# Optimization experiments

Hardware: AMD Instinct MI355X
Metric: run time of the kernel (lower is better)

The kernel has to match this reference:

```python
import jax, jax.numpy as jnp
import numpy as np

B, S, D, H, E, K = 4, 1024, 1024, 4096, 8, 2


def setup_inputs() -> dict:
    key = jax.random.key(0)
    ks = jax.random.split(key, 10)
    s = 0.02
    return {
        "x": jax.random.normal(ks[0], (B, S, D), jnp.float32),
        "noise": jax.random.normal(ks[1], (B, S, E), jnp.float32),
        "Wg": jax.random.normal(ks[2], (D, E), jnp.float32) * s,
        "bg": jnp.zeros((E,), jnp.float32),
        "Wn": jax.random.normal(ks[3], (D, E), jnp.float32) * s,
        "bn": jnp.zeros((E,), jnp.float32),
        "W1": jax.random.normal(ks[4], (E, D, H), jnp.float32) * s,
        "b1": jnp.zeros((E, H), jnp.float32),
        "W2": jax.random.normal(ks[5], (E, H, D), jnp.float32) * s,
        "b2": jnp.zeros((E, D), jnp.float32),
    }


def reference(x, noise, Wg, bg, Wn, bn, W1, b1, W2, b2):
    # --- noisy top-k gating ---
    logits = x @ Wg + bg                                   # [B,S,E]
    noisy = logits + noise * jax.nn.softplus(x @ Wn + bn)  # [B,S,E]
    topk_vals, topk_idx = jax.lax.top_k(noisy, K)          # [B,S,K]
    weights = jax.nn.softmax(topk_vals, axis=-1)           # [B,S,K]
    oh = jax.nn.one_hot(topk_idx, E, dtype=x.dtype)        # [B,S,K,E]
    mask = oh.sum(axis=-2)                                 # [B,S,E] 0/1 (topk idx distinct)
    w_full = (weights[..., None] * oh).sum(axis=-2)        # [B,S,E] combine weights

    # --- per-expert FFN (dense over experts, selected via w_full) ---
    h = jax.nn.gelu(jnp.einsum('bsd,edh->bseh', x, W1) + b1, approximate=False)
    eout = jnp.einsum('bseh,ehd->bsed', h, W2) + b2        # [B,S,E,D]
    combined = jnp.einsum('bse,bsed->bsd', w_full, eout)   # [B,S,D]

    # --- load balancing loss on clean gate probs ---
    gate_probs = jax.nn.softmax(logits, axis=-1)           # [B,S,E]
    expert_count = mask.sum(axis=(0, 1))                   # [E]
    total_tokens = mask.sum()
    expert_util = expert_count / total_tokens
    load_loss = jnp.sum(expert_util * gate_probs.mean(axis=(0, 1))) * E
    return combined, load_loss
```

## Files before the change

kernel.cpp:

```cpp
#include <hip/hip_runtime.h>
#include <hip/hip_bf16.h>

#define T_TOK 4096
#define D_DIM 1024
#define H_DIM 4096
#define E_EXP 8
#define K_TOP 2
#define TP (T_TOK * K_TOP)
#define BM 128
#define BN 128
#define BKS 32
#define MAX_TILES 72

typedef __attribute__((ext_vector_type(8))) short bf16x8;
typedef __attribute__((ext_vector_type(4))) float f32x4;
typedef __attribute__((ext_vector_type(8))) unsigned short u16x8;
typedef __attribute__((ext_vector_type(4))) unsigned short u16x4;

#define SWZ(row, chunk) ((chunk) ^ (((row) >> 1) & 3))

static __device__ __forceinline__ void gload16(const unsigned short* g, unsigned short* l) {
  __builtin_amdgcn_global_load_lds((const __attribute__((address_space(1))) void*)g,
                                   (__attribute__((address_space(3))) void*)l, 16, 0, 0);
}

static __device__ __forceinline__ unsigned short f2bf(float f) {
  unsigned int bits = __float_as_uint(f);
  unsigned int lsb = (bits >> 16) & 1u;
  bits += 0x7fffu + lsb;
  return (unsigned short)(bits >> 16);
}

static __device__ __forceinline__ float gelu_fast(float u) {
  float z = u * (0.79788456080286536f + 0.0356774081f * u * u);
  float t = __expf(-2.f * z);
  return u / (1.f + t);
}

__global__ __launch_bounds__(256) void transpose_bf16_kernel(
    const float* __restrict__ src, unsigned short* __restrict__ dst, int R, int C) {
  __shared__ float tile[64][65];
  const int e = blockIdx.z;
  const int c0 = blockIdx.x * 64, r0 = blockIdx.y * 64;
  const int tid = threadIdx.x;
  const float* s = src + (size_t)e * R * C;
  unsigned short* d = dst + (size_t)e * R * C;

  const int rr = tid >> 4, c4 = tid & 15;
#pragma unroll
  for (int p = 0; p < 4; ++p) {
    int r = rr + p * 16;
    float4 v = *(const float4*)(&s[(size_t)(r0 + r) * C + c0 + c4 * 4]);
    tile[r][c4 * 4 + 0] = v.x;
    tile[r][c4 * 4 + 1] = v.y;
    tile[r][c4 * 4 + 2] = v.z;
    tile[r][c4 * 4 + 3] = v.w;
  }
  __syncthreads();
  const int cc = tid >> 3, r8 = tid & 7;
#pragma unroll
  for (int p = 0; p < 2; ++p) {
    int c = cc + p * 32;
    u16x8 o;
#pragma unroll
    for (int q = 0; q < 8; ++q) o[q] = f2bf(tile[r8 * 8 + q][c]);
    *(u16x8*)(&d[(size_t)(c0 + c) * R + r0 + r8 * 8]) = o;
  }
}

__global__ __launch_bounds__(256) void gating_kernel(
    const float* __restrict__ x, const float* __restrict__ noise,
    const float* __restrict__ Wg, const float* __restrict__ bg,
    const float* __restrict__ Wn, const float* __restrict__ bn,
    int* __restrict__ tok_e, float* __restrict__ tok_w,
    float* __restrict__ gp_tok, int* __restrict__ counts,
    unsigned short* __restrict__ xb) {
  const int tid = threadIdx.x, lane = tid & 63, wid = tid >> 6;
  const int t = blockIdx.x * 4 + wid;
  const float* xrow = x + (size_t)t * D_DIM;
  float ag[8] = {0, 0, 0, 0, 0, 0, 0, 0};
  float an[8] = {0, 0, 0, 0, 0, 0, 0, 0};
#pragma unroll 4
  for (int i = 0; i < 16; ++i) {
    int dd = i * 64 + lane;
    float xv = xrow[dd];
    xb[(size_t)t * D_DIM + dd] = f2bf(xv);
    const float4* g4 = (const float4*)(Wg + (size_t)dd * 8);
    const float4* n4 = (const float4*)(Wn + (size_t)dd * 8);
    float4 ga = g4[0], gb = g4[1], na = n4[0], nb = n4[1];
    ag[0] += xv * ga.x; ag[1] += xv * ga.y; ag[2] += xv * ga.z; ag[3] += xv * ga.w;
    ag[4] += xv * gb.x; ag[5] += xv * gb.y; ag[6] += xv * gb.z; ag[7] += xv * gb.w;
    an[0] += xv * na.x; an[1] += xv * na.y; an[2] += xv * na.z; an[3] += xv * na.w;
    an[4] += xv * nb.x; an[5] += xv * nb.y; an[6] += xv * nb.z; an[7] += xv * nb.w;
  }
#pragma unroll
  for (int e = 0; e < 8; ++e) {
    for (int off = 32; off > 0; off >>= 1) {
      ag[e] += __shfl_down(ag[e], off);
      an[e] += __shfl_down(an[e], off);
    }
  }
  if (lane == 0) {
    float logit[8], noisy[8];
#pragma unroll
    for (int e = 0; e < 8; ++e) {
      logit[e] = ag[e] + bg[e];
      float pre = an[e] + bn[e];
      float sp = fmaxf(pre, 0.f) + log1pf(expf(-fabsf(pre)));
      noisy[e] = logit[e] + noise[(size_t)t * 8 + e] * sp;
    }
    float mx = logit[0];
#pragma unroll
    for (int e = 1; e < 8; ++e) mx = fmaxf(mx, logit[e]);
    float s = 0.f, p[8];
#pragma unroll
    for (int e = 0; e < 8; ++e) { p[e] = expf(logit[e] - mx); s += p[e]; }
    float inv = 1.f / s;
#pragma unroll
    for (int e = 0; e < 8; ++e) gp_tok[(size_t)t * 8 + e] = p[e] * inv;
    int i0 = 0; float v0 = noisy[0];
#pragma unroll
    for (int e = 1; e < 8; ++e) if (noisy[e] > v0) { v0 = noisy[e]; i0 = e; }
    int i1 = -1; float v1 = 0.f;
#pragma unroll
    for (int e = 0; e < 8; ++e) {
      if (e == i0) continue;
      if (i1 < 0 || noisy[e] > v1) { v1 = noisy[e]; i1 = e; }
    }
    float e1 = expf(v1 - v0);
    float w0 = 1.f / (1.f + e1);
    float w1 = e1 * w0;
    tok_e[t * 2 + 0] = i0; tok_e[t * 2 + 1] = i1;
    tok_w[t * 2 + 0] = w0; tok_w[t * 2 + 1] = w1;
    atomicAdd(&counts[i0], 1);
    atomicAdd(&counts[i1], 1);
  }
}

__global__ void scan_kernel(const int* __restrict__ counts, int* __restrict__ offsets,
                            int* __restrict__ cursor, int4* __restrict__ tiles,
                            int* __restrict__ ntiles) {
  if (threadIdx.x == 0 && blockIdx.x == 0) {
    int off = 0, nt = 0;
    for (int e = 0; e < E_EXP; ++e) {
      offsets[e] = off;
      int c = counts[e];
      for (int r = 0; r < c; r += BM) {
        tiles[nt] = make_int4(e, off + r, min(BM, c - r), 0);
        ++nt;
      }
      off += c;
      cursor[e] = 0;
    }
    offsets[E_EXP] = off;
    *ntiles = nt;
  }
}

__global__ __launch_bounds__(256) void scatter_kernel(
    const int* __restrict__ tok_e, const float* __restrict__ tok_w,
    const int* __restrict__ offsets, int* __restrict__ cursor,
    int* __restrict__ pair_token, float* __restrict__ pair_w) {
  int t = blockIdx.x * 256 + threadIdx.x;
  if (t >= T_TOK) return;
#pragma unroll
  for (int k = 0; k < 2; ++k) {
    int e = tok_e[t * 2 + k];
    int pos = atomicAdd(&cursor[e], 1);
    int p = offsets[e] + pos;
    pair_token[p] = t;
    pair_w[p] = tok_w[t * 2 + k];
  }
}

__global__ __launch_bounds__(256) void ffn1_kernel(
    const unsigned short* __restrict__ xb,
    const unsigned short* __restrict__ w1t,
    const float* __restrict__ b1,
    const int* __restrict__ pair_token,
    const int4* __restrict__ tiles, const int* __restrict__ ntiles,
    unsigned short* __restrict__ hbuf) {
  const int NB = H_DIM / BN;
  const int nwg = MAX_TILES * NB;
  int bid = blockIdx.x;
  int wg = (bid & 7) * (nwg >> 3) + (bid >> 3);
  int tileId = wg / NB, nb = wg - tileId * NB;
  if (tileId >= *ntiles) return;
  int4 tl = tiles[tileId];
  const int e = tl.x, row0 = tl.y, rows = tl.z;
  const int n0 = nb * BN;

  __shared__ unsigned short sh[16384];
#define AS1(buf) (sh + (buf) * 4096)
#define BS1(buf) (sh + 8192 + (buf) * 4096)

  const int tid = threadIdx.x;
  const int wid = tid >> 6, lane = tid & 63;
  const int sr = tid >> 2;
  const int sc = tid & 3;
  const int scz = SWZ(sr, sc) * 8;

  int r0a = row0 + sr;       if (r0a > TP - 1) r0a = TP - 1;
  int r1a = row0 + sr + 64;  if (r1a > TP - 1) r1a = TP - 1;
  const unsigned short* a0 = xb + (size_t)pair_token[r0a] * D_DIM + scz;
  const unsigned short* a1 = xb + (size_t)pair_token[r1a] * D_DIM + scz;
  const unsigned short* bp0 = w1t + ((size_t)e * H_DIM + (n0 + sr)) * D_DIM + scz;
  const unsigned short* bp1 = w1t + ((size_t)e * H_DIM + (n0 + sr + 64)) * D_DIM + scz;

  const int wbase = wid * 512;
  const int wr = wid >> 1, wc = wid & 1;
  const int lrow = lane & 15, lkc = lane >> 4;

  f32x4 acc[4][4] = {};

  auto stage = [&](int buf, int k0) {
    gload16(a0 + k0, AS1(buf) + wbase);
    gload16(a1 + k0, AS1(buf) + wbase + 2048);
    gload16(bp0 + k0, BS1(buf) + wbase);
    gload16(bp1 + k0, BS1(buf) + wbase + 2048);
  };
  auto compute_step = [&](int buf) {
    bf16x8 af[4], bfr[4];
#pragma unroll
    for (int m = 0; m < 4; ++m) {
      int r = wr * 64 + m * 16 + lrow;
      af[m] = *(const bf16x8*)(AS1(buf) + r * BKS + SWZ(r, lkc) * 8);
    }
#pragma unroll
    for (int n = 0; n < 4; ++n) {
      int r = wc * 64 + n * 16 + lrow;
      bfr[n] = *(const bf16x8*)(BS1(buf) + r * BKS + SWZ(r, lkc) * 8);
    }
#pragma unroll
    for (int m = 0; m < 4; ++m)
#pragma unroll
      for (int n = 0; n < 4; ++n)
        acc[m][n] = __builtin_amdgcn_mfma_f32_16x16x32_bf16(af[m], bfr[n], acc[m][n], 0, 0, 0);
  };

  const int NK = D_DIM / BKS;
  stage(0, 0);
  stage(1, BKS);
  int cur = 0;
  for (int k = 0; k < NK - 1; ++k) {
    asm volatile("s_waitcnt vmcnt(4)" ::: "memory");
    __builtin_amdgcn_s_barrier();
    __builtin_amdgcn_sched_barrier(0);
    compute_step(cur);
    __builtin_amdgcn_sched_barrier(0);
    __builtin_amdgcn_s_barrier();
    if (k < NK - 2) stage(cur, (k + 2) * BKS);
    cur ^= 1;
  }
  asm volatile("s_waitcnt vmcnt(0)" ::: "memory");
  __builtin_amdgcn_s_barrier();
  __builtin_amdgcn_sched_barrier(0);
  compute_step(cur);

  __syncthreads();
#pragma unroll
  for (int n = 0; n < 4; ++n) {
    int clocal = wc * 64 + n * 16 + lrow;
    float bias = b1[(size_t)e * H_DIM + n0 + clocal];
    int chunk = clocal >> 3, within = clocal & 7;
#pragma unroll
    for (int m = 0; m < 4; ++m) {
#pragma unroll
      for (int j = 0; j < 4; ++j) {
        int rloc = wr * 64 + m * 16 + (lane >> 4) * 4 + j;
        float v = acc[m][n][j] + bias;
        sh[rloc * 128 + ((chunk ^ ((rloc >> 1) & 7)) * 8) + within] = f2bf(gelu_fast(v));
      }
    }
  }
  __syncthreads();
#pragma unroll
  for (int it = 0; it < 8; ++it) {
    int u = tid + 256 * it;
    int r = u >> 4, cg = u & 15;
    if (r < rows) {
      u16x8 v = *(const u16x8*)(&sh[r * 128 + ((cg ^ ((r >> 1) & 7)) * 8)]);
      *(u16x8*)(&hbuf[(size_t)(row0 + r) * H_DIM + n0 + cg * 8]) = v;
    }
  }
#undef AS1
#undef BS1
}

__global__ __launch_bounds__(256) void ffn2_kernel(
    const unsigned short* __restrict__ hbuf,
    const unsigned short* __restrict__ w2t,
    const float* __restrict__ b2,
    const int* __restrict__ pair_token, const float* __restrict__ pair_w,
    const int4* __restrict__ tiles, const int* __restrict__ ntiles,
    float* __restrict__ out) {
  const int NB = D_DIM / BN;
  const int nwg = MAX_TILES * NB;
  int bid = blockIdx.x;
  int wg = (bid & 7) * (nwg >> 3) + (bid >> 3);
  int tileId = wg / NB, nb = wg - tileId * NB;
  if (tileId >= *ntiles) return;
  int4 tl = tiles[tileId];
  const int e = tl.x, row0 = tl.y, rows = tl.z;
  const int n0 = nb * BN;

  __shared__ unsigned short As[2][BM * BKS];
  __shared__ unsigned short Bs[2][BN * BKS];
  __shared__ int stok[BM];
  __shared__ float spw[BM];

  const int tid = threadIdx.x;
  if (tid < BM) {
    int rr = row0 + tid; if (rr > TP - 1) rr = TP - 1;
    stok[tid] = pair_token[rr];
    spw[tid] = pair_w[rr];
  }

  const int wid = tid >> 6, lane = tid & 63;
  const int sr = tid >> 2;
  const int sc = tid & 3;
  const int scz = SWZ(sr, sc) * 8;

  int r0a = row0 + sr;       if (r0a > TP - 1) r0a = TP - 1;
  int r1a = row0 + sr + 64;  if (r1a > TP - 1) r1a = TP - 1;
  const unsigned short* a0 = hbuf + (size_t)r0a * H_DIM + scz;
  const unsigned short* a1 = hbuf + (size_t)r1a * H_DIM + scz;
  const unsigned short* bp0 = w2t + ((size_t)e * D_DIM + (n0 + sr)) * H_DIM + scz;
  const unsigned short* bp1 = w2t + ((size_t)e * D_DIM + (n0 + sr + 64)) * H_DIM + scz;

  const int wbase = wid * 512;
  const int wr = wid >> 1, wc = wid & 1;
  const int lrow = lane & 15, lkc = lane >> 4;

  f32x4 acc[4][4] = {};

  auto stage = [&](int buf, int k0) {
    gload16(a0 + k0, &As[buf][wbase]);
    gload16(a1 + k0, &As[buf][wbase + 2048]);
    gload16(bp0 + k0, &Bs[buf][wbase]);
    gload16(bp1 + k0, &Bs[buf][wbase + 2048]);
  };
  auto compute_step = [&](int buf) {
    bf16x8 af[4], bfr[4];
#pragma unroll
    for (int m = 0; m < 4; ++m) {
      int r = wr * 64 + m * 16 + lrow;
      af[m] = *(const bf16x8*)(&As[buf][r * BKS + SWZ(r, lkc) * 8]);
    }
#pragma unroll
    for (int n = 0; n < 4; ++n) {
      int r = wc * 64 + n * 16 + lrow;
      bfr[n] = *(const bf16x8*)(&Bs[buf][r * BKS + SWZ(r, lkc) * 8]);
    }
#pragma unroll
    for (int m = 0; m < 4; ++m)
#pragma unroll
      for (int n = 0; n < 4; ++n)
        acc[m][n] = __builtin_amdgcn_mfma_f32_16x16x32_bf16(af[m], bfr[n], acc[m][n], 0, 0, 0);
  };

  const int NK = H_DIM / BKS;
  stage(0, 0);
  stage(1, BKS);
  int cur = 0;
  for (int k = 0; k < NK - 1; ++k) {
    asm volatile("s_waitcnt vmcnt(4)" ::: "memory");
    __builtin_amdgcn_s_barrier();
    __builtin_amdgcn_sched_barrier(0);
    compute_step(cur);
    __builtin_amdgcn_sched_barrier(0);
    __builtin_amdgcn_s_barrier();
    if (k < NK - 2) stage(cur, (k + 2) * BKS);
    cur ^= 1;
  }
  asm volatile("s_waitcnt vmcnt(0)" ::: "memory");
  __builtin_amdgcn_s_barrier();
  __builtin_amdgcn_sched_barrier(0);
  compute_step(cur);

  const int colbase = n0 + wc * 64;
#pragma unroll
  for (int n = 0; n < 4; ++n) {
    int colg = colbase + n * 16 + lrow;
    float bias = b2[(size_t)e * D_DIM + colg];
#pragma unroll
    for (int m = 0; m < 4; ++m) {
      int rbase = wr * 64 + m * 16 + (lane >> 4) * 4;
#pragma unroll
      for (int j = 0; j < 4; ++j) {
        int rloc = rbase + j;
        if (rloc < rows) {
          float v = acc[m][n][j] + bias;
          unsafeAtomicAdd(&out[(size_t)stok[rloc] * D_DIM + colg], spw[rloc] * v);
        }
      }
    }
  }
}

__global__ __launch_bounds__(256) void loss_kernel(
    const float* __restrict__ gp_tok, const int* __restrict__ counts,
    float* __restrict__ out) {
  __shared__ float red[256];
  const int tid = threadIdx.x;
  float part[8] = {0, 0, 0, 0, 0, 0, 0, 0};
  for (int r = tid; r < T_TOK; r += 256) {
    const float* g = gp_tok + (size_t)r * 8;
#pragma unroll
    for (int e = 0; e < 8; ++e) part[e] += g[e];
  }
  float total[8];
#pragma unroll
  for (int e = 0; e < 8; ++e) {
    red[tid] = part[e];
    __syncthreads();
    for (int s = 128; s > 0; s >>= 1) {
      if (tid < s) red[tid] += red[tid + s];
      __syncthreads();
    }
    if (tid == 0) total[e] = red[0];
    __syncthreads();
  }
  if (tid == 0) {
    float ll = 0.f;
#pragma unroll
    for (int e = 0; e < 8; ++e)
      ll += ((float)counts[e] / (float)TP) * (total[e] / (float)T_TOK);
    out[(size_t)T_TOK * D_DIM] = ll * (float)E_EXP;
  }
}

extern "C" void kernel_launch(void* const* d_in, const int* in_sizes, int n_in,
                              void* d_out, int out_size, void* d_ws, size_t ws_size,
                              hipStream_t stream) {
  (void)in_sizes; (void)n_in; (void)ws_size;
  const float* x     = (const float*)d_in[0];
  const float* noise = (const float*)d_in[1];
  const float* Wg    = (const float*)d_in[2];
  const float* bg    = (const float*)d_in[3];
  const float* Wn    = (const float*)d_in[4];
  const float* bn    = (const float*)d_in[5];
  const float* W1    = (const float*)d_in[6];
  const float* b1    = (const float*)d_in[7];
  const float* W2    = (const float*)d_in[8];
  const float* b2    = (const float*)d_in[9];
  float* out = (float*)d_out;

  char* ws = (char*)d_ws;
  size_t o = 0;
  auto take = [&](size_t b) { size_t r = o; o += (b + 255) & ~(size_t)255; return r; };
  int*   counts     = (int*)(ws + take(16 * 4));
  int*   cursor     = counts + 8;
  int*   offsets    = (int*)(ws + take(9 * 4));
  int*   ntiles     = (int*)(ws + take(4));
  int4*  tiles      = (int4*)(ws + take(MAX_TILES * 16));
  int*   tok_e      = (int*)(ws + take((size_t)TP * 4));
  float* tok_w      = (float*)(ws + take((size_t)TP * 4));
  float* gp_tok     = (float*)(ws + take((size_t)T_TOK * 8 * 4));
  int*   pair_token = (int*)(ws + take((size_t)TP * 4));
  float* pair_w     = (float*)(ws + take((size_t)TP * 4));
  unsigned short* xb  = (unsigned short*)(ws + take((size_t)T_TOK * D_DIM * 2));
  unsigned short* w1t = (unsigned short*)(ws + take((size_t)E_EXP * H_DIM * D_DIM * 2));
  unsigned short* w2t = (unsigned short*)(ws + take((size_t)E_EXP * H_DIM * D_DIM * 2));
  unsigned short* hbuf = (unsigned short*)(ws + take((size_t)TP * H_DIM * 2));

  hipMemsetAsync(d_out, 0, (size_t)out_size * sizeof(float), stream);
  hipMemsetAsync(counts, 0, 16 * 4, stream);

  transpose_bf16_kernel<<<dim3(H_DIM / 64, D_DIM / 64, E_EXP), 256, 0, stream>>>(
      W1, w1t, D_DIM, H_DIM);
  transpose_bf16_kernel<<<dim3(D_DIM / 64, H_DIM / 64, E_EXP), 256, 0, stream>>>(
      W2, w2t, H_DIM, D_DIM);
  gating_kernel<<<T_TOK / 4, 256, 0, stream>>>(x, noise, Wg, bg, Wn, bn,
                                               tok_e, tok_w, gp_tok, counts, xb);
  scan_kernel<<<1, 64, 0, stream>>>(counts, offsets, cursor, tiles, ntiles);
  scatter_kernel<<<T_TOK / 256, 256, 0, stream>>>(tok_e, tok_w, offsets, cursor,
                                                  pair_token, pair_w);
  ffn1_kernel<<<dim3(MAX_TILES * (H_DIM / BN)), 256, 0, stream>>>(
      xb, w1t, b1, pair_token, tiles, ntiles, hbuf);
  ffn2_kernel<<<dim3(MAX_TILES * (D_DIM / BN)), 256, 0, stream>>>(
      hbuf, w2t, b2, pair_token, pair_w, tiles, ntiles, out);
  loss_kernel<<<1, 256, 0, stream>>>(gp_tok, counts, out);
}
```

Before: 476.1 us.

## Split ffn2 K reduction across two 256-thread groups per block

Doubles the ffn2 block to 512 threads and gives each half of the block its own half of the H reduction dimension, with separate double-buffered LDS tiles. Both halves accumulate independently and atomically add their partial results to the output, with only the first half adding the bias. This aims to raise the number of waves in flight for the small grid of ffn2 tiles and shorten each block's serial K loop. The cost is double the LDS per block, twice the atomic traffic to the output, and block-wide barriers that now synchronise both halves.

```diff
diff --git a/kernel.cpp b/kernel.cpp
--- a/kernel.cpp
+++ b/kernel.cpp
@@ -287,7 +287,7 @@
 #undef BS1
 }
 
-__global__ __launch_bounds__(256) void ffn2_kernel(
+__global__ __launch_bounds__(512) void ffn2_kernel(
     const unsigned short* __restrict__ hbuf,
     const unsigned short* __restrict__ w2t,
     const float* __restrict__ b2,
@@ -304,8 +304,8 @@
   const int e = tl.x, row0 = tl.y, rows = tl.z;
   const int n0 = nb * BN;
 
-  __shared__ unsigned short As[2][BM * BKS];
-  __shared__ unsigned short Bs[2][BN * BKS];
+  __shared__ unsigned short As[2][2][BM * BKS];
+  __shared__ unsigned short Bs[2][2][BN * BKS];
   __shared__ int stok[BM];
   __shared__ float spw[BM];
 
@@ -316,41 +316,44 @@
     spw[tid] = pair_w[rr];
   }
 
-  const int wid = tid >> 6, lane = tid & 63;
-  const int sr = tid >> 2;
+  const int g = tid >> 8;
+  const int t4 = tid & 255;
+  const int wid4 = t4 >> 6, lane = tid & 63;
+  const int sr = t4 >> 2;
   const int sc = tid & 3;
   const int scz = SWZ(sr, sc) * 8;
+  const int kbase = g * (H_DIM / 2);
 
   int r0a = row0 + sr;       if (r0a > TP - 1) r0a = TP - 1;
   int r1a = row0 + sr + 64;  if (r1a > TP - 1) r1a = TP - 1;
-  const unsigned short* a0 = hbuf + (size_t)r0a * H_DIM + scz;
-  const unsigned short* a1 = hbuf + (size_t)r1a * H_DIM + scz;
-  const unsigned short* bp0 = w2t + ((size_t)e * D_DIM + (n0 + sr)) * H_DIM + scz;
-  const unsigned short* bp1 = w2t + ((size_t)e * D_DIM + (n0 + sr + 64)) * H_DIM + scz;
-
-  const int wbase = wid * 512;
-  const int wr = wid >> 1, wc = wid & 1;
+  const unsigned short* a0 = hbuf + (size_t)r0a * H_DIM + kbase + scz;
+  const unsigned short* a1 = hbuf + (size_t)r1a * H_DIM + kbase + scz;
+  const unsigned short* bp0 = w2t + ((size_t)e * D_DIM + (n0 + sr)) * H_DIM + kbase + scz;
+  const unsigned short* bp1 = w2t + ((size_t)e * D_DIM + (n0 + sr + 64)) * H_DIM + kbase + scz;
+
+  const int wbase = wid4 * 512;
+  const int wr = wid4 >> 1, wc = wid4 & 1;
   const int lrow = lane & 15, lkc = lane >> 4;
 
   f32x4 acc[4][4] = {};
 
   auto stage = [&](int buf, int k0) {
-    gload16(a0 + k0, &As[buf][wbase]);
-    gload16(a1 + k0, &As[buf][wbase + 2048]);
-    gload16(bp0 + k0, &Bs[buf][wbase]);
-    gload16(bp1 + k0, &Bs[buf][wbase + 2048]);
+    gload16(a0 + k0, &As[g][buf][wbase]);
+    gload16(a1 + k0, &As[g][buf][wbase + 2048]);
+    gload16(bp0 + k0, &Bs[g][buf][wbase]);
+    gload16(bp1 + k0, &Bs[g][buf][wbase + 2048]);
   };
   auto compute_step = [&](int buf) {
     bf16x8 af[4], bfr[4];
 #pragma unroll
     for (int m = 0; m < 4; ++m) {
       int r = wr * 64 + m * 16 + lrow;
-      af[m] = *(const bf16x8*)(&As[buf][r * BKS + SWZ(r, lkc) * 8]);
+      af[m] = *(const bf16x8*)(&As[g][buf][r * BKS + SWZ(r, lkc) * 8]);
     }
 #pragma unroll
     for (int n = 0; n < 4; ++n) {
       int r = wc * 64 + n * 16 + lrow;
-      bfr[n] = *(const bf16x8*)(&Bs[buf][r * BKS + SWZ(r, lkc) * 8]);
+      bfr[n] = *(const bf16x8*)(&Bs[g][buf][r * BKS + SWZ(r, lkc) * 8]);
     }
 #pragma unroll
     for (int m = 0; m < 4; ++m)
@@ -359,7 +362,7 @@
         acc[m][n] = __builtin_amdgcn_mfma_f32_16x16x32_bf16(af[m], bfr[n], acc[m][n], 0, 0, 0);
   };
 
-  const int NK = H_DIM / BKS;
+  const int NK = (H_DIM / 2) / BKS;
   stage(0, 0);
   stage(1, BKS);
   int cur = 0;
@@ -382,7 +385,7 @@
 #pragma unroll
   for (int n = 0; n < 4; ++n) {
     int colg = colbase + n * 16 + lrow;
-    float bias = b2[(size_t)e * D_DIM + colg];
+    float bias = (g == 0) ? b2[(size_t)e * D_DIM + colg] : 0.f;
 #pragma unroll
     for (int m = 0; m < 4; ++m) {
       int rbase = wr * 64 + m * 16 + (lane >> 4) * 4;
@@ -478,7 +481,7 @@
                                                   pair_token, pair_w);
   ffn1_kernel<<<dim3(MAX_TILES * (H_DIM / BN)), 256, 0, stream>>>(
       xb, w1t, b1, pair_token, tiles, ntiles, hbuf);
-  ffn2_kernel<<<dim3(MAX_TILES * (D_DIM / BN)), 256, 0, stream>>>(
+  ffn2_kernel<<<dim3(MAX_TILES * (D_DIM / BN)), 512, 0, stream>>>(
       hbuf, w2t, b2, pair_token, pair_w, tiles, ntiles, out);
   loss_kernel<<<1, 256, 0, stream>>>(gp_tok, counts, out);
 }
```

Measured after the change: 564.2 us. 1.18x slower.

## Enlarge FFN1 tiles to 256 rows with 512-thread workgroups

Applied to the files above, without the earlier changes.

The first expert GEMM moves from 128x128 tiles with 4 waves to 256x128 tiles with 8 waves. A separate 256-row tile list is built in the scan kernel, and the LDS A buffer is doubled. Each W1 tile staged into LDS is now reused across twice as many token rows, which cuts weight traffic and the number of workgroups. The cost is more LDS per block, lower occupancy, and extra padding waste on partial tiles per expert.

```diff
diff --git a/kernel.cpp b/kernel.cpp
--- a/kernel.cpp
+++ b/kernel.cpp
@@ -9,8 +9,10 @@
 #define TP (T_TOK * K_TOP)
 #define BM 128
 #define BN 128
+#define BM1 256
 #define BKS 32
 #define MAX_TILES 72
+#define MAX_T256 48
 
 typedef __attribute__((ext_vector_type(8))) short bf16x8;
 typedef __attribute__((ext_vector_type(4))) float f32x4;
@@ -139,9 +141,10 @@
 
 __global__ void scan_kernel(const int* __restrict__ counts, int* __restrict__ offsets,
                             int* __restrict__ cursor, int4* __restrict__ tiles,
-                            int* __restrict__ ntiles) {
+                            int* __restrict__ ntiles, int4* __restrict__ tiles256,
+                            int* __restrict__ nt256) {
   if (threadIdx.x == 0 && blockIdx.x == 0) {
-    int off = 0, nt = 0;
+    int off = 0, nt = 0, n2 = 0;
     for (int e = 0; e < E_EXP; ++e) {
       offsets[e] = off;
       int c = counts[e];
@@ -149,11 +152,16 @@
         tiles[nt] = make_int4(e, off + r, min(BM, c - r), 0);
         ++nt;
       }
+      for (int r = 0; r < c; r += BM1) {
+        tiles256[n2] = make_int4(e, off + r, min(BM1, c - r), 0);
+        ++n2;
+      }
       off += c;
       cursor[e] = 0;
     }
     offsets[E_EXP] = off;
     *ntiles = nt;
+    *nt256 = n2;
   }
 }
 
@@ -173,51 +181,50 @@
   }
 }
 
-__global__ __launch_bounds__(256) void ffn1_kernel(
+__global__ __launch_bounds__(512, 4) void ffn1_kernel(
     const unsigned short* __restrict__ xb,
     const unsigned short* __restrict__ w1t,
     const float* __restrict__ b1,
     const int* __restrict__ pair_token,
-    const int4* __restrict__ tiles, const int* __restrict__ ntiles,
+    const int4* __restrict__ tiles256, const int* __restrict__ nt256,
     unsigned short* __restrict__ hbuf) {
   const int NB = H_DIM / BN;
-  const int nwg = MAX_TILES * NB;
+  const int nwg = MAX_T256 * NB;
   int bid = blockIdx.x;
   int wg = (bid & 7) * (nwg >> 3) + (bid >> 3);
   int tileId = wg / NB, nb = wg - tileId * NB;
-  if (tileId >= *ntiles) return;
-  int4 tl = tiles[tileId];
+  if (tileId >= *nt256) return;
+  int4 tl = tiles256[tileId];
   const int e = tl.x, row0 = tl.y, rows = tl.z;
   const int n0 = nb * BN;
 
-  __shared__ unsigned short sh[16384];
-#define AS1(buf) (sh + (buf) * 4096)
-#define BS1(buf) (sh + 8192 + (buf) * 4096)
+  __shared__ unsigned short sh[32768];
+#define AS1(buf) (sh + (buf) * 8192)
+#define BS1(buf) (sh + 16384 + (buf) * 4096)
 
   const int tid = threadIdx.x;
   const int wid = tid >> 6, lane = tid & 63;
   const int sr = tid >> 2;
   const int sc = tid & 3;
-  const int scz = SWZ(sr, sc) * 8;
-
-  int r0a = row0 + sr;       if (r0a > TP - 1) r0a = TP - 1;
-  int r1a = row0 + sr + 64;  if (r1a > TP - 1) r1a = TP - 1;
-  const unsigned short* a0 = xb + (size_t)pair_token[r0a] * D_DIM + scz;
-  const unsigned short* a1 = xb + (size_t)pair_token[r1a] * D_DIM + scz;
-  const unsigned short* bp0 = w1t + ((size_t)e * H_DIM + (n0 + sr)) * D_DIM + scz;
-  const unsigned short* bp1 = w1t + ((size_t)e * H_DIM + (n0 + sr + 64)) * D_DIM + scz;
-
-  const int wbase = wid * 512;
+
+  int ra0 = row0 + sr;        if (ra0 > TP - 1) ra0 = TP - 1;
+  int ra1 = row0 + sr + 128;  if (ra1 > TP - 1) ra1 = TP - 1;
+  const unsigned short* a0 = xb + (size_t)pair_token[ra0] * D_DIM + SWZ(sr, sc) * 8;
+  const unsigned short* a1 = xb + (size_t)pair_token[ra1] * D_DIM + SWZ(sr + 128, sc) * 8;
+  const unsigned short* bp = w1t + ((size_t)e * H_DIM + (n0 + sr)) * D_DIM + SWZ(sr, sc) * 8;
+
+  const int wbase = wid * 128;
+  const int ldso = wid * 512;
+
   const int wr = wid >> 1, wc = wid & 1;
   const int lrow = lane & 15, lkc = lane >> 4;
 
   f32x4 acc[4][4] = {};
 
   auto stage = [&](int buf, int k0) {
-    gload16(a0 + k0, AS1(buf) + wbase);
-    gload16(a1 + k0, AS1(buf) + wbase + 2048);
-    gload16(bp0 + k0, BS1(buf) + wbase);
-    gload16(bp1 + k0, BS1(buf) + wbase + 2048);
+    gload16(a0 + k0, AS1(buf) + ldso);
+    gload16(a1 + k0, AS1(buf) + 4096 + ldso);
+    gload16(bp + k0, BS1(buf) + ldso);
   };
   auto compute_step = [&](int buf) {
     bf16x8 af[4], bfr[4];
@@ -243,7 +250,7 @@
   stage(1, BKS);
   int cur = 0;
   for (int k = 0; k < NK - 1; ++k) {
-    asm volatile("s_waitcnt vmcnt(4)" ::: "memory");
+    asm volatile("s_waitcnt vmcnt(3)" ::: "memory");
     __builtin_amdgcn_s_barrier();
     __builtin_amdgcn_sched_barrier(0);
     compute_step(cur);
@@ -260,9 +267,9 @@
   __syncthreads();
 #pragma unroll
   for (int n = 0; n < 4; ++n) {
-    int clocal = wc * 64 + n * 16 + lrow;
-    float bias = b1[(size_t)e * H_DIM + n0 + clocal];
-    int chunk = clocal >> 3, within = clocal & 7;
+    int cl = wc * 64 + n * 16 + lrow;
+    float bias = b1[(size_t)e * H_DIM + n0 + cl];
+    int chunk = cl >> 3, within = cl & 7;
 #pragma unroll
     for (int m = 0; m < 4; ++m) {
 #pragma unroll
@@ -276,7 +283,7 @@
   __syncthreads();
 #pragma unroll
   for (int it = 0; it < 8; ++it) {
-    int u = tid + 256 * it;
+    int u = tid + 512 * it;
     int r = u >> 4, cg = u & 15;
     if (r < rows) {
       u16x8 v = *(const u16x8*)(&sh[r * 128 + ((cg ^ ((r >> 1) & 7)) * 8)]);
@@ -285,6 +292,7 @@
   }
 #undef AS1
 #undef BS1
+  (void)wbase;
 }
 
 __global__ __launch_bounds__(256) void ffn2_kernel(
@@ -453,7 +461,9 @@
   int*   cursor     = counts + 8;
   int*   offsets    = (int*)(ws + take(9 * 4));
   int*   ntiles     = (int*)(ws + take(4));
+  int*   nt256      = (int*)(ws + take(4));
   int4*  tiles      = (int4*)(ws + take(MAX_TILES * 16));
+  int4*  tiles256   = (int4*)(ws + take(MAX_T256 * 16));
   int*   tok_e      = (int*)(ws + take((size_t)TP * 4));
   float* tok_w      = (float*)(ws + take((size_t)TP * 4));
   float* gp_tok     = (float*)(ws + take((size_t)T_TOK * 8 * 4));
@@ -473,11 +483,12 @@
       W2, w2t, H_DIM, D_DIM);
   gating_kernel<<<T_TOK / 4, 256, 0, stream>>>(x, noise, Wg, bg, Wn, bn,
                                                tok_e, tok_w, gp_tok, counts, xb);
-  scan_kernel<<<1, 64, 0, stream>>>(counts, offsets, cursor, tiles, ntiles);
+  scan_kernel<<<1, 64, 0, stream>>>(counts, offsets, cursor, tiles, ntiles,
+                                    tiles256, nt256);
   scatter_kernel<<<T_TOK / 256, 256, 0, stream>>>(tok_e, tok_w, offsets, cursor,
                                                   pair_token, pair_w);
-  ffn1_kernel<<<dim3(MAX_TILES * (H_DIM / BN)), 256, 0, stream>>>(
-      xb, w1t, b1, pair_token, tiles, ntiles, hbuf);
+  ffn1_kernel<<<dim3(MAX_T256 * (H_DIM / BN)), 512, 0, stream>>>(
+      xb, w1t, b1, pair_token, tiles256, nt256, hbuf);
   ffn2_kernel<<<dim3(MAX_TILES * (D_DIM / BN)), 256, 0, stream>>>(
       hbuf, w2t, b2, pair_token, pair_w, tiles, ntiles, out);
   loss_kernel<<<1, 256, 0, stream>>>(gp_tok, counts, out);
```

Result: slower. 498.9 us (+4.8%).

## Merge gating and weight transposes into one launch; fuse scan, scatter and loss

Applied to the files above, without the earlier changes.

Gating and both bf16 weight-transpose kernels now run as one grid, with each block picking its role from its index. Scan, scatter and load-loss are folded into one single-block finalize kernel that keeps offsets and cursors in shared memory. This cuts the launch count from eight to four and lets the gating work overlap the transposes. The cost is that the scatter runs serially in one block of 256 threads instead of 16 blocks, and the loss reduction now follows that scatter inside the same block.

```diff
diff --git a/kernel.cpp b/kernel.cpp
--- a/kernel.cpp
+++ b/kernel.cpp
@@ -37,12 +37,100 @@
   return u / (1.f + t);
 }
 
-__global__ __launch_bounds__(256) void transpose_bf16_kernel(
-    const float* __restrict__ src, unsigned short* __restrict__ dst, int R, int C) {
+#define NGATE (T_TOK / 4)
+#define NTR1  ((H_DIM / 64) * (D_DIM / 64) * E_EXP)
+#define NTR2  ((D_DIM / 64) * (H_DIM / 64) * E_EXP)
+
+__global__ __launch_bounds__(256) void front_kernel(
+    const float* __restrict__ W1, unsigned short* __restrict__ w1t,
+    const float* __restrict__ W2, unsigned short* __restrict__ w2t,
+    const float* __restrict__ x, const float* __restrict__ noise,
+    const float* __restrict__ Wg, const float* __restrict__ bg,
+    const float* __restrict__ Wn, const float* __restrict__ bn,
+    int* __restrict__ tok_e, float* __restrict__ tok_w,
+    float* __restrict__ gp_tok, int* __restrict__ counts,
+    unsigned short* __restrict__ xb) {
   __shared__ float tile[64][65];
-  const int e = blockIdx.z;
-  const int c0 = blockIdx.x * 64, r0 = blockIdx.y * 64;
+  int bid = blockIdx.x;
   const int tid = threadIdx.x;
+
+  if (bid < NGATE) {
+    const int lane = tid & 63, wid = tid >> 6;
+    const int t = bid * 4 + wid;
+    const float* xrow = x + (size_t)t * D_DIM;
+    float ag[8] = {0, 0, 0, 0, 0, 0, 0, 0};
+    float an[8] = {0, 0, 0, 0, 0, 0, 0, 0};
+#pragma unroll 4
+    for (int i = 0; i < 16; ++i) {
+      int dd = i * 64 + lane;
+      float xv = xrow[dd];
+      xb[(size_t)t * D_DIM + dd] = f2bf(xv);
+      const float4* g4 = (const float4*)(Wg + (size_t)dd * 8);
+      const float4* n4 = (const float4*)(Wn + (size_t)dd * 8);
+      float4 ga = g4[0], gb = g4[1], na = n4[0], nb = n4[1];
+      ag[0] += xv * ga.x; ag[1] += xv * ga.y; ag[2] += xv * ga.z; ag[3] += xv * ga.w;
+      ag[4] += xv * gb.x; ag[5] += xv * gb.y; ag[6] += xv * gb.z; ag[7] += xv * gb.w;
+      an[0] += xv * na.x; an[1] += xv * na.y; an[2] += xv * na.z; an[3] += xv * na.w;
+      an[4] += xv * nb.x; an[5] += xv * nb.y; an[6] += xv * nb.z; an[7] += xv * nb.w;
+    }
+#pragma unroll
+    for (int e = 0; e < 8; ++e) {
+      for (int off = 32; off > 0; off >>= 1) {
+        ag[e] += __shfl_down(ag[e], off);
+        an[e] += __shfl_down(an[e], off);
+      }
+    }
+    if (lane == 0) {
+      float logit[8], noisy[8];
+#pragma unroll
+      for (int e = 0; e < 8; ++e) {
+        logit[e] = ag[e] + bg[e];
+        float pre = an[e] + bn[e];
+        float sp = fmaxf(pre, 0.f) + log1pf(expf(-fabsf(pre)));
+        noisy[e] = logit[e] + noise[(size_t)t * 8 + e] * sp;
+      }
+      float mx = logit[0];
+#pragma unroll
+      for (int e = 1; e < 8; ++e) mx = fmaxf(mx, logit[e]);
+      float s = 0.f, p[8];
+#pragma unroll
+      for (int e = 0; e < 8; ++e) { p[e] = expf(logit[e] - mx); s += p[e]; }
+      float inv = 1.f / s;
+#pragma unroll
+      for (int e = 0; e < 8; ++e) gp_tok[(size_t)t * 8 + e] = p[e] * inv;
+      int i0 = 0; float v0 = noisy[0];
+#pragma unroll
+      for (int e = 1; e < 8; ++e) if (noisy[e] > v0) { v0 = noisy[e]; i0 = e; }
+      int i1 = -1; float v1 = 0.f;
+#pragma unroll
+      for (int e = 0; e < 8; ++e) {
+        if (e == i0) continue;
+        if (i1 < 0 || noisy[e] > v1) { v1 = noisy[e]; i1 = e; }
+      }
+      float e1 = expf(v1 - v0);
+      float w0 = 1.f / (1.f + e1);
+      float w1 = e1 * w0;
+      tok_e[t * 2 + 0] = i0; tok_e[t * 2 + 1] = i1;
+      tok_w[t * 2 + 0] = w0; tok_w[t * 2 + 1] = w1;
+      atomicAdd(&counts[i0], 1);
+      atomicAdd(&counts[i1], 1);
+    }
+    return;
+  }
+  bid -= NGATE;
+
+  const float* src; unsigned short* dst; int R, C, bx, by, e;
+  if (bid < NTR1) {
+    R = D_DIM; C = H_DIM;
+    bx = bid & 63; by = (bid >> 6) & 15; e = bid >> 10;
+    src = W1; dst = w1t;
+  } else {
+    bid -= NTR1;
+    R = H_DIM; C = D_DIM;
+    bx = bid & 15; by = (bid >> 4) & 63; e = bid >> 10;
+    src = W2; dst = w2t;
+  }
+  const int c0 = bx * 64, r0 = by * 64;
   const float* s = src + (size_t)e * R * C;
   unsigned short* d = dst + (size_t)e * R * C;
 
@@ -68,108 +156,68 @@
   }
 }
 
-__global__ __launch_bounds__(256) void gating_kernel(
-    const float* __restrict__ x, const float* __restrict__ noise,
-    const float* __restrict__ Wg, const float* __restrict__ bg,
-    const float* __restrict__ Wn, const float* __restrict__ bn,
-    int* __restrict__ tok_e, float* __restrict__ tok_w,
-    float* __restrict__ gp_tok, int* __restrict__ counts,
-    unsigned short* __restrict__ xb) {
-  const int tid = threadIdx.x, lane = tid & 63, wid = tid >> 6;
-  const int t = blockIdx.x * 4 + wid;
-  const float* xrow = x + (size_t)t * D_DIM;
-  float ag[8] = {0, 0, 0, 0, 0, 0, 0, 0};
-  float an[8] = {0, 0, 0, 0, 0, 0, 0, 0};
-#pragma unroll 4
-  for (int i = 0; i < 16; ++i) {
-    int dd = i * 64 + lane;
-    float xv = xrow[dd];
-    xb[(size_t)t * D_DIM + dd] = f2bf(xv);
-    const float4* g4 = (const float4*)(Wg + (size_t)dd * 8);
-    const float4* n4 = (const float4*)(Wn + (size_t)dd * 8);
-    float4 ga = g4[0], gb = g4[1], na = n4[0], nb = n4[1];
-    ag[0] += xv * ga.x; ag[1] += xv * ga.y; ag[2] += xv * ga.z; ag[3] += xv * ga.w;
-    ag[4] += xv * gb.x; ag[5] += xv * gb.y; ag[6] += xv * gb.z; ag[7] += xv * gb.w;
-    an[0] += xv * na.x; an[1] += xv * na.y; an[2] += xv * na.z; an[3] += xv * na.w;
-    an[4] += xv * nb.x; an[5] += xv * nb.y; an[6] += xv * nb.z; an[7] += xv * nb.w;
-  }
-#pragma unroll
-  for (int e = 0; e < 8; ++e) {
-    for (int off = 32; off > 0; off >>= 1) {
-      ag[e] += __shfl_down(ag[e], off);
-      an[e] += __shfl_down(an[e], off);
-    }
-  }
-  if (lane == 0) {
-    float logit[8], noisy[8];
-#pragma unroll
-    for (int e = 0; e < 8; ++e) {
-      logit[e] = ag[e] + bg[e];
-      float pre = an[e] + bn[e];
-      float sp = fmaxf(pre, 0.f) + log1pf(expf(-fabsf(pre)));
-      noisy[e] = logit[e] + noise[(size_t)t * 8 + e] * sp;
-    }
-    float mx = logit[0];
-#pragma unroll
-    for (int e = 1; e < 8; ++e) mx = fmaxf(mx, logit[e]);
-    float s = 0.f, p[8];
-#pragma unroll
-    for (int e = 0; e < 8; ++e) { p[e] = expf(logit[e] - mx); s += p[e]; }
-    float inv = 1.f / s;
-#pragma unroll
-    for (int e = 0; e < 8; ++e) gp_tok[(size_t)t * 8 + e] = p[e] * inv;
-    int i0 = 0; float v0 = noisy[0];
-#pragma unroll
-    for (int e = 1; e < 8; ++e) if (noisy[e] > v0) { v0 = noisy[e]; i0 = e; }
-    int i1 = -1; float v1 = 0.f;
-#pragma unroll
-    for (int e = 0; e < 8; ++e) {
-      if (e == i0) continue;
-      if (i1 < 0 || noisy[e] > v1) { v1 = noisy[e]; i1 = e; }
-    }
-    float e1 = expf(v1 - v0);
-    float w0 = 1.f / (1.f + e1);
-    float w1 = e1 * w0;
-    tok_e[t * 2 + 0] = i0; tok_e[t * 2 + 1] = i1;
-    tok_w[t * 2 + 0] = w0; tok_w[t * 2 + 1] = w1;
-    atomicAdd(&counts[i0], 1);
-    atomicAdd(&counts[i1], 1);
-  }
-}
-
-__global__ void scan_kernel(const int* __restrict__ counts, int* __restrict__ offsets,
-                            int* __restrict__ cursor, int4* __restrict__ tiles,
-                            int* __restrict__ ntiles) {
-  if (threadIdx.x == 0 && blockIdx.x == 0) {
+__global__ __launch_bounds__(256) void finalize_kernel(
+    const int* __restrict__ counts, int4* __restrict__ tiles,
+    int* __restrict__ ntiles,
+    const int* __restrict__ tok_e, const float* __restrict__ tok_w,
+    int* __restrict__ pair_token, float* __restrict__ pair_w,
+    const float* __restrict__ gp_tok, float* __restrict__ out) {
+  __shared__ int s_off[E_EXP];
+  __shared__ int s_cur[E_EXP];
+  __shared__ float red[256];
+  const int tid = threadIdx.x;
+
+  if (tid == 0) {
     int off = 0, nt = 0;
     for (int e = 0; e < E_EXP; ++e) {
-      offsets[e] = off;
+      s_off[e] = off;
       int c = counts[e];
       for (int r = 0; r < c; r += BM) {
         tiles[nt] = make_int4(e, off + r, min(BM, c - r), 0);
         ++nt;
       }
       off += c;
-      cursor[e] = 0;
-    }
-    offsets[E_EXP] = off;
+    }
     *ntiles = nt;
   }
-}
-
-__global__ __launch_bounds__(256) void scatter_kernel(
-    const int* __restrict__ tok_e, const float* __restrict__ tok_w,
-    const int* __restrict__ offsets, int* __restrict__ cursor,
-    int* __restrict__ pair_token, float* __restrict__ pair_w) {
-  int t = blockIdx.x * 256 + threadIdx.x;
-  if (t >= T_TOK) return;
-#pragma unroll
-  for (int k = 0; k < 2; ++k) {
-    int e = tok_e[t * 2 + k];
-    int pos = atomicAdd(&cursor[e], 1);
-    int p = offsets[e] + pos;
-    pair_token[p] = t;
-    pair_w[p] = tok_w[t * 2 + k];
+  if (tid < E_EXP) s_cur[tid] = 0;
+  __syncthreads();
+
+  for (int t = tid; t < T_TOK; t += 256) {
+#pragma unroll
+    for (int k = 0; k < 2; ++k) {
+      int e = tok_e[t * 2 + k];
+      int pos = atomicAdd(&s_cur[e], 1);
+      int p = s_off[e] + pos;
+      pair_token[p] = t;
+      pair_w[p] = tok_w[t * 2 + k];
+    }
+  }
+
+  float part[8] = {0, 0, 0, 0, 0, 0, 0, 0};
+  for (int r = tid; r < T_TOK; r += 256) {
+    const float* g = gp_tok + (size_t)r * 8;
+#pragma unroll
+    for (int e = 0; e < 8; ++e) part[e] += g[e];
+  }
+  float total[8];
+#pragma unroll
+  for (int e = 0; e < 8; ++e) {
+    red[tid] = part[e];
+    __syncthreads();
+    for (int s = 128; s > 0; s >>= 1) {
+      if (tid < s) red[tid] += red[tid + s];
+      __syncthreads();
+    }
+    if (tid == 0) total[e] = red[0];
+    __syncthreads();
+  }
+  if (tid == 0) {
+    float ll = 0.f;
+#pragma unroll
+    for (int e = 0; e < 8; ++e)
+      ll += ((float)counts[e] / (float)TP) * (total[e] / (float)T_TOK);
+    out[(size_t)T_TOK * D_DIM] = ll * (float)E_EXP;
   }
 }
 
@@ -398,38 +446,6 @@
   }
 }
 
-__global__ __launch_bounds__(256) void loss_kernel(
-    const float* __restrict__ gp_tok, const int* __restrict__ counts,
-    float* __restrict__ out) {
-  __shared__ float red[256];
-  const int tid = threadIdx.x;
-  float part[8] = {0, 0, 0, 0, 0, 0, 0, 0};
-  for (int r = tid; r < T_TOK; r += 256) {
-    const float* g = gp_tok + (size_t)r * 8;
-#pragma unroll
-    for (int e = 0; e < 8; ++e) part[e] += g[e];
-  }
-  float total[8];
-#pragma unroll
-  for (int e = 0; e < 8; ++e) {
-    red[tid] = part[e];
-    __syncthreads();
-    for (int s = 128; s > 0; s >>= 1) {
-      if (tid < s) red[tid] += red[tid + s];
-      __syncthreads();
-    }
-    if (tid == 0) total[e] = red[0];
-    __syncthreads();
-  }
-  if (tid == 0) {
-    float ll = 0.f;
-#pragma unroll
-    for (int e = 0; e < 8; ++e)
-      ll += ((float)counts[e] / (float)TP) * (total[e] / (float)T_TOK);
-    out[(size_t)T_TOK * D_DIM] = ll * (float)E_EXP;
-  }
-}
-
 extern "C" void kernel_launch(void* const* d_in, const int* in_sizes, int n_in,
                               void* d_out, int out_size, void* d_ws, size_t ws_size,
                               hipStream_t stream) {
@@ -450,8 +466,6 @@
   size_t o = 0;
   auto take = [&](size_t b) { size_t r = o; o += (b + 255) & ~(size_t)255; return r; };
   int*   counts     = (int*)(ws + take(16 * 4));
-  int*   cursor     = counts + 8;
-  int*   offsets    = (int*)(ws + take(9 * 4));
   int*   ntiles     = (int*)(ws + take(4));
   int4*  tiles      = (int4*)(ws + take(MAX_TILES * 16));
   int*   tok_e      = (int*)(ws + take((size_t)TP * 4));
@@ -467,18 +481,13 @@
   hipMemsetAsync(d_out, 0, (size_t)out_size * sizeof(float), stream);
   hipMemsetAsync(counts, 0, 16 * 4, stream);
 
-  transpose_bf16_kernel<<<dim3(H_DIM / 64, D_DIM / 64, E_EXP), 256, 0, stream>>>(
-      W1, w1t, D_DIM, H_DIM);
-  transpose_bf16_kernel<<<dim3(D_DIM / 64, H_DIM / 64, E_EXP), 256, 0, stream>>>(
-      W2, w2t, H_DIM, D_DIM);
-  gating_kernel<<<T_TOK / 4, 256, 0, stream>>>(x, noise, Wg, bg, Wn, bn,
-                                               tok_e, tok_w, gp_tok, counts, xb);
-  scan_kernel<<<1, 64, 0, stream>>>(counts, offsets, cursor, tiles, ntiles);
-  scatter_kernel<<<T_TOK / 256, 256, 0, stream>>>(tok_e, tok_w, offsets, cursor,
-                                                  pair_token, pair_w);
+  front_kernel<<<NGATE + NTR1 + NTR2, 256, 0, stream>>>(
+      W1, w1t, W2, w2t, x, noise, Wg, bg, Wn, bn,
+      tok_e, tok_w, gp_tok, counts, xb);
+  finalize_kernel<<<1, 256, 0, stream>>>(counts, tiles, ntiles, tok_e, tok_w,
+                                         pair_token, pair_w, gp_tok, out);
   ffn1_kernel<<<dim3(MAX_TILES * (H_DIM / BN)), 256, 0, stream>>>(
       xb, w1t, b1, pair_token, tiles, ntiles, hbuf);
   ffn2_kernel<<<dim3(MAX_TILES * (D_DIM / BN)), 256, 0, stream>>>(
       hbuf, w2t, b2, pair_token, pair_w, tiles, ntiles, out);
-  loss_kernel<<<1, 256, 0, stream>>>(gp_tok, counts, out);
-}
+}
```

New measurement: 437.2 us. 8.2% less time.
